# Optimization experiments

Hardware: AMD Instinct MI355X
Metric: run time of the kernel (lower is better)

## Reference

```python
import jax, jax.numpy as jnp
import numpy as np

H = 16      # how_many_heads
DH = 64     # dimension_of_head
D_K = 1024  # dimension_of_key (input dim); scaler = sqrt(D_K), faithful to source
NEG = -np.finfo(np.float32).max


def setup_inputs() -> dict:
    key0 = jax.random.key(0)
    ks = jax.random.split(key0, 8)
    B, S, D = 2, 2048, 1024
    query = jax.random.normal(ks[0], (B, S, D), dtype=jnp.float32)
    key_in = jax.random.normal(ks[1], (B, S, D), dtype=jnp.float32)
    value = jax.random.normal(ks[2], (B, S, D), dtype=jnp.float32)
    mask = jax.random.bernoulli(ks[3], 0.5, (B, S, S))  # bool, True = masked
    # nn.Linear(in, out, bias=False): y = x @ W^T with W:[out,in]; store [in,out] directly
    sc = 1.0 / np.sqrt(D)
    W_q = jax.random.normal(ks[4], (D, H * DH), dtype=jnp.float32) * sc
    W_k = jax.random.normal(ks[5], (D, H * DH), dtype=jnp.float32) * sc
    W_v = jax.random.normal(ks[6], (D, H * DH), dtype=jnp.float32) * sc
    W_o = jax.random.normal(ks[7], (H * DH, D), dtype=jnp.float32) * sc
    return {"query": query, "key": key_in, "value": value, "mask": mask,
            "W_q": W_q, "W_k": W_k, "W_v": W_v, "W_o": W_o}


def reference(query, key, value, mask, W_q, W_k, W_v, W_o):
    B, Sq, _ = query.shape
    # project and split heads: [B, S, H, DH] -> [B, H, S, DH]
    q = (query @ W_q).reshape(B, Sq, H, DH).transpose(0, 2, 1, 3)
    k = (key @ W_k).reshape(B, -1, H, DH).transpose(0, 2, 1, 3)
    v = (value @ W_v).reshape(B, -1, H, DH).transpose(0, 2, 1, 3)
    # scores: [B, H, Sq, Sk], scaled by sqrt(dimension_of_key)=sqrt(D_K)
    scores = jnp.einsum('bhqd,bhkd->bhqk', q, k) / np.float32(np.sqrt(D_K))
    # mask: [B, Sq, Sk] -> [B, H, Sq, Sk]; masked_fill with -finfo(float32).max
    scores = jnp.where(mask[:, None, :, :], NEG, scores)
    # FAITHFUL to source: softmax over dim=2 (the QUERY axis of the 4D tensor)
    attn = jax.nn.softmax(scores, axis=2)
    hidden = jnp.einsum('bhqk,bhkd->bhqd', attn, v)  # [B, H, Sq, DH]
    hidden = hidden.transpose(0, 2, 1, 3).reshape(B, Sq, H * DH) @ W_o
    return hidden, k, v
```

## Files before the change

### kernel.cpp

```cpp
#include <hip/hip_runtime.h>
#include <hip/hip_bf16.h>

#define BB 2
#define SS 2048
#define DD 1024
#define HH 16
#define DHH 64

#define SCLOG2E 0.045084221f

typedef unsigned short u16;
typedef unsigned int   u32;
typedef __bf16 bf16_t;
typedef bf16_t bf16x8 __attribute__((ext_vector_type(8)));
typedef u16    u16x8  __attribute__((ext_vector_type(8)));
typedef u32    u32x4v __attribute__((ext_vector_type(4)));
typedef float  f32x4  __attribute__((ext_vector_type(4)));

#define MFMA(a,b,c) __builtin_amdgcn_mfma_f32_16x16x32_bf16(a,b,c,0,0,0)

#define SW(c,r)  ((c) ^ ((r) & 7))
#define SW3(c,r) ((c) ^ ((r) & 3))

typedef __attribute__((address_space(1))) const unsigned int as1_u32;
typedef __attribute__((address_space(3))) unsigned int as3_u32;

__device__ __forceinline__ void gld16(const void* g, void* l){
  __builtin_amdgcn_global_load_lds((as1_u32*)g, (as3_u32*)l, 16, 0, 0);
}

__device__ __forceinline__ u16 f2bf(float f){
  u32 u = __builtin_bit_cast(u32, f);
  u32 r = (u + 0x7fffu + ((u >> 16) & 1u)) >> 16;
  return (u16)r;
}
__device__ __forceinline__ u16 nbf(float f){
  bf16_t b = (bf16_t)f;
  return __builtin_bit_cast(u16, b);
}
__device__ __forceinline__ float bf2f(u16 v){
  u32 u = ((u32)v) << 16;
  return __builtin_bit_cast(float, u);
}
__device__ __forceinline__ bf16x8 ldb8(const u16* p){
  return __builtin_bit_cast(bf16x8, *(const u16x8*)p);
}

__device__ __forceinline__ void stage64(const u16* __restrict__ g0, int stride,
                                        u16* lds0, int tid){
  int w = tid >> 6, lane = tid & 63;
  #pragma unroll
  for (int j = 0; j < 2; j++){
    int slot = j*256 + w*64 + lane;
    int row = slot >> 3, c = slot & 7;
    gld16(g0 + (size_t)row*stride + (SW(c,row) << 3),
          lds0 + (size_t)(j*256 + w*64)*8);
  }
}

__device__ __forceinline__ void stage32(const u16* __restrict__ g0, int stride,
                                        u16* lds0, int tid){
  int w = tid >> 6, lane = tid & 63;
  #pragma unroll
  for (int j = 0; j < 2; j++){
    int slot = j*256 + w*64 + lane;
    int row = slot >> 2, c = slot & 3;
    gld16(g0 + (size_t)row*stride + (SW3(c,row) << 3),
          lds0 + (size_t)(j*256 + w*64)*8);
  }
}

__global__ __launch_bounds__(256) void cvt3(const float* __restrict__ s0,
                                            const float* __restrict__ s1,
                                            const float* __restrict__ s2,
                                            u16* __restrict__ d0,
                                            u16* __restrict__ d1,
                                            u16* __restrict__ d2){
  const float* s = blockIdx.z == 0 ? s0 : (blockIdx.z == 1 ? s1 : s2);
  u16*         d = blockIdx.z == 0 ? d0 : (blockIdx.z == 1 ? d1 : d2);
  size_t i = ((size_t)blockIdx.x*256 + threadIdx.x) * 8;
  const float4* p = (const float4*)(s + i);
  float4 x = p[0], y = p[1];
  u16x8 u;
  u[0]=f2bf(x.x); u[1]=f2bf(x.y); u[2]=f2bf(x.z); u[3]=f2bf(x.w);
  u[4]=f2bf(y.x); u[5]=f2bf(y.y); u[6]=f2bf(y.z); u[7]=f2bf(y.w);
  *(u16x8*)(d + i) = u;
}

__global__ __launch_bounds__(256) void detect_mask(const u32* mw, u32* flag){
  __shared__ int fBig, fFloat;
  if (threadIdx.x == 0){ fBig = 0; fFloat = 0; }
  __syncthreads();
  for (int i = threadIdx.x; i < 4096; i += 256){
    u32 w = mw[i];
    if (w == 0x3f800000u) fFloat = 1;
    else if (w > 1u) fBig = 1;
  }
  __syncthreads();
  if (threadIdx.x == 0) *flag = fFloat ? 2u : (fBig ? 1u : 0u);
}

__global__ __launch_bounds__(256) void pack_mask(const void* __restrict__ mask,
                                                 const u32* __restrict__ flag,
                                                 u32* __restrict__ pm){
  int w = blockIdx.x * 256 + threadIdx.x;
  if (w >= BB*SS*(SS/32)) return;
  u32 f = *flag;
  size_t e0 = (size_t)w * 32;
  u32 bits = 0;
  if (f == 1u){
    const uchar4* mb = (const uchar4*)((const unsigned char*)mask + e0);
    #pragma unroll
    for (int j = 0; j < 8; j++){
      uchar4 v = mb[j];
      bits |= (v.x?1u:0u) << (4*j)   | (v.y?1u:0u) << (4*j+1)
            | (v.z?1u:0u) << (4*j+2) | (v.w?1u:0u) << (4*j+3);
    }
  } else if (f == 0u){
    const int4* mi = (const int4*)((const int*)mask + e0);
    #pragma unroll
    for (int j = 0; j < 8; j++){
      int4 v = mi[j];
      bits |= (v.x?1u:0u) << (4*j)   | (v.y?1u:0u) << (4*j+1)
            | (v.z?1u:0u) << (4*j+2) | (v.w?1u:0u) << (4*j+3);
    }
  } else {
    const float4* mf = (const float4*)((const float*)mask + e0);
    #pragma unroll
    for (int j = 0; j < 8; j++){
      float4 v = mf[j];
      bits |= (v.x!=0.f?1u:0u) << (4*j)   | (v.y!=0.f?1u:0u) << (4*j+1)
            | (v.z!=0.f?1u:0u) << (4*j+2) | (v.w!=0.f?1u:0u) << (4*j+3);
    }
  }
  pm[w] = bits;
}

__global__ __launch_bounds__(256) void prep_w(const float* __restrict__ W0,
                                              const float* __restrict__ W1,
                                              const float* __restrict__ W2,
                                              const float* __restrict__ W3,
                                              u16* __restrict__ Wt){
  const float* Ws[4] = {W0, W1, W2, W3};
  const float* W = Ws[blockIdx.z];
  float scl = (blockIdx.z == 0) ? SCLOG2E : 1.0f;
  u16* O = Wt + (size_t)blockIdx.z * DD * DD;
  __shared__ float tile[64][65];
  int kb = blockIdx.x * 64, nb = blockIdx.y * 64;
  int col = threadIdx.x & 63, rr = threadIdx.x >> 6;
  #pragma unroll
  for (int i = 0; i < 16; i++){
    int row = i*4 + rr;
    tile[row][col] = W[(size_t)(kb+row)*DD + nb + col];
  }
  __syncthreads();
  #pragma unroll
  for (int i = 0; i < 16; i++){
    int row = i*4 + rr;
    O[(size_t)(nb+row)*DD + kb + col] = f2bf(tile[col][row] * scl);
  }
}

struct GA { const u16* A; const u16* Bt; u16* Cb; float* Co; int mode; };

__global__ __launch_bounds__(256) void gemm32(GA a0, GA a1, GA a2){
  GA ga = blockIdx.z == 0 ? a0 : (blockIdx.z == 1 ? a1 : a2);
  __shared__ u16 As[2][128*32];
  __shared__ u16 Bs[2][128*32];
  int mb = blockIdx.x * 128, nb = blockIdx.y * 128;
  int tid = threadIdx.x, w = tid >> 6, lane = tid & 63, ln = lane & 15, g = lane >> 4;
  int wr = w >> 1, wc = w & 1;
  f32x4 acc[4][4];
  #pragma unroll
  for (int i = 0; i < 4; i++)
    #pragma unroll
    for (int j = 0; j < 4; j++) acc[i][j] = (f32x4){0,0,0,0};

  stage32(ga.A  + (size_t)mb*DD, DD, As[0], tid);
  stage32(ga.Bt + (size_t)nb*DD, DD, Bs[0], tid);
  __syncthreads();
  int buf = 0;
  for (int t = 0; t < 32; t++){
    if (t < 31){
      stage32(ga.A  + (size_t)mb*DD + (t+1)*32, DD, As[buf^1], tid);
      stage32(ga.Bt + (size_t)nb*DD + (t+1)*32, DD, Bs[buf^1], tid);
    }
    bf16x8 av[4], bv[4];
    #pragma unroll
    for (int mf = 0; mf < 4; mf++){
      int row = wr*64 + mf*16 + ln;
      av[mf] = ldb8(&As[buf][row*32 + (SW3(g,row) << 3)]);
    }
    #pragma unroll
    for (int nf = 0; nf < 4; nf++){
      int row = wc*64 + nf*16 + ln;
      bv[nf] = ldb8(&Bs[buf][row*32 + (SW3(g,row) << 3)]);
    }
    #pragma unroll
    for (int mf = 0; mf < 4; mf++)
      #pragma unroll
      for (int nf = 0; nf < 4; nf++)
        acc[mf][nf] = MFMA(av[mf], bv[nf], acc[mf][nf]);
    __syncthreads();
    buf ^= 1;
  }
  #pragma unroll
  for (int mf = 0; mf < 4; mf++){
    #pragma unroll
    for (int nf = 0; nf < 4; nf++){
      #pragma unroll
      for (int r = 0; r < 4; r++){
        int row = mb + wr*64 + mf*16 + g*4 + r;
        int col = nb + wc*64 + nf*16 + ln;
        float v = acc[mf][nf][r];
        if (ga.mode != 2)
          ga.Cb[(size_t)row*DD + col] = f2bf(v);
        if (ga.mode == 1){
          int b_ = row >> 11, s_ = row & (SS-1);
          int h_ = col >> 6,  d_ = col & 63;
          ga.Co[(((size_t)(b_*HH + h_))*SS + s_)*DHH + d_] = v;
        }
        if (ga.mode == 2)
          ga.Co[(size_t)row*DD + col] = v;
      }
    }
  }
}

__global__ __launch_bounds__(256) void pass1_sum(const u16* __restrict__ Qb,
                                                 const u16* __restrict__ Kb,
                                                 const u32* __restrict__ pm,
                                                 float* __restrict__ cO){
  __shared__ u16 Qst[2][64*64];
  int b = blockIdx.z, h = blockIdx.y;
  int kblk = blockIdx.x * 64;
  int tid = threadIdx.x, w = tid >> 6, lane = tid & 63, ln = lane & 15, g = lane >> 4;
  const u16* kp = Kb + ((size_t)b*SS + kblk + w*16 + ln)*DD + h*DHH + g*8;
  bf16x8 kf0 = ldb8(kp), kf1 = ldb8(kp + 32);
  float cr[4] = {0,0,0,0};

  stage64(Qb + ((size_t)b*SS)*DD + h*DHH, DD, Qst[0], tid);
  __syncthreads();
  int buf = 0;
  size_t kword = (size_t)(b*SS)*(SS/32) + ((kblk + w*16) >> 5);
  int ksh = (w & 1) * 16 + g*4;
  for (int t = 0; t < 32; t++){
    if (t < 31) stage64(Qb + ((size_t)b*SS + (t+1)*64)*DD + h*DHH, DD, Qst[buf^1], tid);
    #pragma unroll
    for (int qc = 0; qc < 4; qc++){
      int row = qc*16 + ln;
      bf16x8 b0 = ldb8(&Qst[buf][row*64 + (SW(g,  row) << 3)]);
      bf16x8 b1 = ldb8(&Qst[buf][row*64 + (SW(g+4,row) << 3)]);
      int q = t*64 + qc*16 + ln;
      f32x4 sf = {0,0,0,0};
      sf = MFMA(kf0, b0, sf);
      sf = MFMA(kf1, b1, sf);
      u32 mw = pm[(size_t)q*(SS/32) + kword];
      #pragma unroll
      for (int r = 0; r < 4; r++){
        float e = __builtin_amdgcn_exp2f(sf[r]);
        cr[r] += ((mw >> (ksh + r)) & 1u) ? 0.f : e;
      }
    }
    __syncthreads();
    buf ^= 1;
  }
  #pragma unroll
  for (int r = 0; r < 4; r++){
    #pragma unroll
    for (int msk = 1; msk < 16; msk <<= 1)
      cr[r] += __shfl_xor(cr[r], msk, 64);
  }
  if (ln == 0){
    #pragma unroll
    for (int r = 0; r < 4; r++)
      cO[((size_t)b*HH + h)*SS + kblk + w*16 + g*4 + r] = cr[r];
  }
}

__global__ __launch_bounds__(256) void scale_v(const u16* __restrict__ Vb,
                                               const float* __restrict__ cI,
                                               u16* __restrict__ Vt){
  int b = blockIdx.z, h = blockIdx.y;
  int st = blockIdx.x * 64;
  __shared__ u16 tile[64][72];
  int col = threadIdx.x & 63, rr = threadIdx.x >> 6;
  #pragma unroll
  for (int i = 0; i < 16; i++){
    int row = i*4 + rr;
    int s = st + row;
    float inv = 1.0f / cI[((size_t)b*HH + h)*SS + s];
    float v = bf2f(Vb[((size_t)b*SS + s)*DD + h*DHH + col]);
    tile[row][col] = f2bf(v * inv);
  }
  __syncthreads();
  int pc = (col & 32) + ((col >> 2) & 3)*8 + ((col >> 4) & 1)*4 + (col & 3);
  #pragma unroll
  for (int i = 0; i < 16; i++){
    int row = i*4 + rr;
    Vt[(((size_t)b*HH + h)*DHH + row)*SS + st + pc] = tile[col][row];
  }
}

__global__ __launch_bounds__(256) void pass2_pv(const u16* __restrict__ Qb,
                                                const u16* __restrict__ Kb,
                                                const u16* __restrict__ Vt,
                                                const u32* __restrict__ pm,
                                                u16* __restrict__ Hb){
  __shared__ u16 Kst[2][64*64];
  __shared__ u16 Vst[2][64*64];
  int b = blockIdx.z, h = blockIdx.y;
  int qt = blockIdx.x * 64;
  int tid = threadIdx.x, w = tid >> 6, lane = tid & 63, ln = lane & 15, g = lane >> 4;
  int qrow = qt + w*16 + ln;
  const u16* qp = Qb + ((size_t)b*SS + qrow)*DD + h*DHH + g*8;
  bf16x8 qf0 = ldb8(qp), qf1 = ldb8(qp + 32);
  f32x4 acc[4];
  #pragma unroll
  for (int d = 0; d < 4; d++) acc[d] = (f32x4){0,0,0,0};

  const u16* Kg  = Kb + ((size_t)b*SS)*DD + h*DHH;
  const u16* Vth = Vt + ((size_t)b*HH + h)*DHH*SS;
  const u32* pmrow = pm + ((size_t)b*SS + qrow)*(SS/32);

  stage64(Kg,  DD, Kst[0], tid);
  stage64(Vth, SS, Vst[0], tid);
  __syncthreads();
  int buf = 0;
  for (int t = 0; t < 32; t++){
    if (t < 31){
      stage64(Kg + (size_t)(t+1)*64*DD, DD, Kst[buf^1], tid);
      stage64(Vth + (t+1)*64,           SS, Vst[buf^1], tid);
    }
    u32 mlo = pmrow[t*2], mhi = pmrow[t*2 + 1];
    u32 pk[8];
    #pragma unroll
    for (int kc = 0; kc < 4; kc++){
      int row = kc*16 + ln;
      bf16x8 a0 = ldb8(&Kst[buf][row*64 + (SW(g,  row) << 3)]);
      bf16x8 a1 = ldb8(&Kst[buf][row*64 + (SW(g+4,row) << 3)]);
      f32x4 sf = {0,0,0,0};
      sf = MFMA(a0, qf0, sf);
      sf = MFMA(a1, qf1, sf);
      u32 mword = (kc < 2) ? mlo : mhi;
      int msh = (kc & 1) * 16 + g*4;
      float p0 = ((mword >> (msh+0)) & 1u) ? 0.f : __builtin_amdgcn_exp2f(sf[0]);
      float p1 = ((mword >> (msh+1)) & 1u) ? 0.f : __builtin_amdgcn_exp2f(sf[1]);
      float p2 = ((mword >> (msh+2)) & 1u) ? 0.f : __builtin_amdgcn_exp2f(sf[2]);
      float p3 = ((mword >> (msh+3)) & 1u) ? 0.f : __builtin_amdgcn_exp2f(sf[3]);
      pk[kc*2]   = (u32)nbf(p0) | ((u32)nbf(p1) << 16);
      pk[kc*2+1] = (u32)nbf(p2) | ((u32)nbf(p3) << 16);
    }
    #pragma unroll
    for (int kh = 0; kh < 2; kh++){
      bf16x8 pa = __builtin_bit_cast(bf16x8,
        (u32x4v){pk[4*kh], pk[4*kh+1], pk[4*kh+2], pk[4*kh+3]});
      #pragma unroll
      for (int df = 0; df < 4; df++){
        int row = df*16 + ln;
        bf16x8 bv = ldb8(&Vst[buf][row*64 + (SW(kh*4+g, row) << 3)]);
        acc[df] = MFMA(pa, bv, acc[df]);
      }
    }
    __syncthreads();
    buf ^= 1;
  }
  #pragma unroll
  for (int df = 0; df < 4; df++)
    #pragma unroll
    for (int r = 0; r < 4; r++){
      int row = qt + w*16 + g*4 + r;
      int col = h*DHH + df*16 + ln;
      Hb[((size_t)b*SS + row)*DD + col] = f2bf(acc[df][r]);
    }
}

extern "C" void kernel_launch(void* const* d_in, const int* in_sizes, int n_in,
                              void* d_out, int out_size, void* d_ws, size_t ws_size,
                              hipStream_t stream){
  (void)in_sizes; (void)n_in; (void)out_size; (void)ws_size;
  const float* query = (const float*)d_in[0];
  const float* key   = (const float*)d_in[1];
  const float* value = (const float*)d_in[2];
  const void*  mask  = d_in[3];
  const float* W_q = (const float*)d_in[4];
  const float* W_k = (const float*)d_in[5];
  const float* W_v = (const float*)d_in[6];
  const float* W_o = (const float*)d_in[7];

  float* out   = (float*)d_out;
  float* out_h = out;
  float* out_k = out   + (size_t)BB*HH*SS*DHH;
  float* out_v = out_k + (size_t)BB*HH*SS*DHH;

  char* w = (char*)d_ws;
  u16*   Wt  = (u16*)(w);
  u16*   Av  = (u16*)(w + (size_t)( 8u<<20));
  u16*   Qb  = (u16*)(w + (size_t)(16u<<20));
  u16*   Kb  = (u16*)(w + (size_t)(24u<<20));
  u16*   Vb  = (u16*)(w + (size_t)(32u<<20));
  u16*   Vt  = (u16*)(w + (size_t)(40u<<20));
  float* cS  = (float*)(w + (size_t)(48u<<20));
  u32*   pm  = (u32*)(w + (size_t)(48u<<20) + (512u<<10));
  u32*   flag= (u32*)(w + (size_t)(48u<<20) + (1664u<<10));
  u16*   Hb  = Av;
  u16*   Aq  = (u16*)out_h;
  u16*   Ak  = Aq + (size_t)BB*SS*DD;

  detect_mask<<<dim3(1), dim3(256), 0, stream>>>((const u32*)mask, flag);
  pack_mask<<<dim3(1024), dim3(256), 0, stream>>>(mask, flag, pm);
  prep_w<<<dim3(16,16,4), dim3(256), 0, stream>>>(W_q, W_k, W_v, W_o, Wt);

  cvt3<<<dim3(2048,1,3), dim3(256), 0, stream>>>(query, key, value, Aq, Ak, Av);

  GA gq = { Aq, Wt,             Qb, nullptr, 0 };
  GA gk = { Ak, Wt + 1*1048576, Kb, out_k,   1 };
  GA gv = { Av, Wt + 2*1048576, Vb, out_v,   1 };
  gemm32<<<dim3(32,8,3), dim3(256), 0, stream>>>(gq, gk, gv);

  pass1_sum<<<dim3(SS/64, HH, BB), dim3(256), 0, stream>>>(Qb, Kb, pm, cS);
  scale_v<<<dim3(SS/64, HH, BB), dim3(256), 0, stream>>>(Vb, cS, Vt);
  pass2_pv<<<dim3(SS/64, HH, BB), dim3(256), 0, stream>>>(Qb, Kb, Vt, pm, Hb);

  GA go = { Hb, Wt + 3*1048576, nullptr, out_h, 2 };
  gemm32<<<dim3(32,8,1), dim3(256), 0, stream>>>(go, go, go);
}
```

Measured before the change: 245.5 us.

## Deepen GEMM K-tile to 64 and double key rows per pass1 block

The projection and output GEMMs now stage 64-wide K slices instead of 32, which halves the number of loop iterations and barriers and doubles the MFMA work between syncs. The column-sum pass now handles 128 keys per block, with each wave holding two K fragments. Each staged Q tile and mask word is therefore reused for twice as many keys, halving Q re-streaming from global memory. The cost is more LDS per GEMM block (64 KB), more registers, and half as many pass1 blocks, which can reduce occupancy.

Result: faster. 229.8 us (-6.4%).

```diff
diff --git a/kernel.cpp b/kernel.cpp
--- a/kernel.cpp
+++ b/kernel.cpp
@@ -58,14 +58,14 @@
   }
 }
 
-__device__ __forceinline__ void stage32(const u16* __restrict__ g0, int stride,
-                                        u16* lds0, int tid){
+__device__ __forceinline__ void stage128(const u16* __restrict__ g0, int stride,
+                                         u16* lds0, int tid){
   int w = tid >> 6, lane = tid & 63;
   #pragma unroll
-  for (int j = 0; j < 2; j++){
+  for (int j = 0; j < 4; j++){
     int slot = j*256 + w*64 + lane;
-    int row = slot >> 2, c = slot & 3;
-    gld16(g0 + (size_t)row*stride + (SW3(c,row) << 3),
+    int row = slot >> 3, c = slot & 7;
+    gld16(g0 + (size_t)row*stride + (SW(c,row) << 3),
           lds0 + (size_t)(j*256 + w*64)*8);
   }
 }
@@ -163,10 +163,10 @@
 
 struct GA { const u16* A; const u16* Bt; u16* Cb; float* Co; int mode; };
 
-__global__ __launch_bounds__(256) void gemm32(GA a0, GA a1, GA a2){
+__global__ __launch_bounds__(256) void gemm64(GA a0, GA a1, GA a2){
   GA ga = blockIdx.z == 0 ? a0 : (blockIdx.z == 1 ? a1 : a2);
-  __shared__ u16 As[2][128*32];
-  __shared__ u16 Bs[2][128*32];
+  __shared__ u16 As[2][128*64];
+  __shared__ u16 Bs[2][128*64];
   int mb = blockIdx.x * 128, nb = blockIdx.y * 128;
   int tid = threadIdx.x, w = tid >> 6, lane = tid & 63, ln = lane & 15, g = lane >> 4;
   int wr = w >> 1, wc = w & 1;
@@ -176,31 +176,35 @@
     #pragma unroll
     for (int j = 0; j < 4; j++) acc[i][j] = (f32x4){0,0,0,0};
 
-  stage32(ga.A  + (size_t)mb*DD, DD, As[0], tid);
-  stage32(ga.Bt + (size_t)nb*DD, DD, Bs[0], tid);
+  stage128(ga.A  + (size_t)mb*DD, DD, As[0], tid);
+  stage128(ga.Bt + (size_t)nb*DD, DD, Bs[0], tid);
   __syncthreads();
   int buf = 0;
-  for (int t = 0; t < 32; t++){
-    if (t < 31){
-      stage32(ga.A  + (size_t)mb*DD + (t+1)*32, DD, As[buf^1], tid);
-      stage32(ga.Bt + (size_t)nb*DD + (t+1)*32, DD, Bs[buf^1], tid);
-    }
-    bf16x8 av[4], bv[4];
+  for (int t = 0; t < 16; t++){
+    if (t < 15){
+      stage128(ga.A  + (size_t)mb*DD + (t+1)*64, DD, As[buf^1], tid);
+      stage128(ga.Bt + (size_t)nb*DD + (t+1)*64, DD, Bs[buf^1], tid);
+    }
+    bf16x8 av[4][2], bv[4][2];
     #pragma unroll
     for (int mf = 0; mf < 4; mf++){
       int row = wr*64 + mf*16 + ln;
-      av[mf] = ldb8(&As[buf][row*32 + (SW3(g,row) << 3)]);
+      av[mf][0] = ldb8(&As[buf][row*64 + (SW(g,  row) << 3)]);
+      av[mf][1] = ldb8(&As[buf][row*64 + (SW(g+4,row) << 3)]);
     }
     #pragma unroll
     for (int nf = 0; nf < 4; nf++){
       int row = wc*64 + nf*16 + ln;
-      bv[nf] = ldb8(&Bs[buf][row*32 + (SW3(g,row) << 3)]);
+      bv[nf][0] = ldb8(&Bs[buf][row*64 + (SW(g,  row) << 3)]);
+      bv[nf][1] = ldb8(&Bs[buf][row*64 + (SW(g+4,row) << 3)]);
     }
     #pragma unroll
     for (int mf = 0; mf < 4; mf++)
       #pragma unroll
-      for (int nf = 0; nf < 4; nf++)
-        acc[mf][nf] = MFMA(av[mf], bv[nf], acc[mf][nf]);
+      for (int nf = 0; nf < 4; nf++){
+        acc[mf][nf] = MFMA(av[mf][0], bv[nf][0], acc[mf][nf]);
+        acc[mf][nf] = MFMA(av[mf][1], bv[nf][1], acc[mf][nf]);
+      }
     __syncthreads();
     buf ^= 1;
   }
@@ -233,17 +237,20 @@
                                                  float* __restrict__ cO){
   __shared__ u16 Qst[2][64*64];
   int b = blockIdx.z, h = blockIdx.y;
-  int kblk = blockIdx.x * 64;
+  int kblk = blockIdx.x * 128;
   int tid = threadIdx.x, w = tid >> 6, lane = tid & 63, ln = lane & 15, g = lane >> 4;
-  const u16* kp = Kb + ((size_t)b*SS + kblk + w*16 + ln)*DD + h*DHH + g*8;
-  bf16x8 kf0 = ldb8(kp), kf1 = ldb8(kp + 32);
-  float cr[4] = {0,0,0,0};
+  bf16x8 kf[2][2];
+  #pragma unroll
+  for (int f = 0; f < 2; f++){
+    const u16* kp = Kb + ((size_t)b*SS + kblk + w*32 + f*16 + ln)*DD + h*DHH + g*8;
+    kf[f][0] = ldb8(kp); kf[f][1] = ldb8(kp + 32);
+  }
+  float cr[2][4] = {{0,0,0,0},{0,0,0,0}};
 
   stage64(Qb + ((size_t)b*SS)*DD + h*DHH, DD, Qst[0], tid);
   __syncthreads();
   int buf = 0;
-  size_t kword = (size_t)(b*SS)*(SS/32) + ((kblk + w*16) >> 5);
-  int ksh = (w & 1) * 16 + g*4;
+  size_t kwbase = (size_t)(b*SS)*(SS/32) + (kblk >> 5) + w;
   for (int t = 0; t < 32; t++){
     if (t < 31) stage64(Qb + ((size_t)b*SS + (t+1)*64)*DD + h*DHH, DD, Qst[buf^1], tid);
     #pragma unroll
@@ -252,29 +259,36 @@
       bf16x8 b0 = ldb8(&Qst[buf][row*64 + (SW(g,  row) << 3)]);
       bf16x8 b1 = ldb8(&Qst[buf][row*64 + (SW(g+4,row) << 3)]);
       int q = t*64 + qc*16 + ln;
-      f32x4 sf = {0,0,0,0};
-      sf = MFMA(kf0, b0, sf);
-      sf = MFMA(kf1, b1, sf);
-      u32 mw = pm[(size_t)q*(SS/32) + kword];
-      #pragma unroll
-      for (int r = 0; r < 4; r++){
-        float e = __builtin_amdgcn_exp2f(sf[r]);
-        cr[r] += ((mw >> (ksh + r)) & 1u) ? 0.f : e;
+      u32 mw = pm[(size_t)q*(SS/32) + kwbase];
+      #pragma unroll
+      for (int f = 0; f < 2; f++){
+        f32x4 sf = {0,0,0,0};
+        sf = MFMA(kf[f][0], b0, sf);
+        sf = MFMA(kf[f][1], b1, sf);
+        #pragma unroll
+        for (int r = 0; r < 4; r++){
+          float e = __builtin_amdgcn_exp2f(sf[r]);
+          cr[f][r] += ((mw >> (f*16 + g*4 + r)) & 1u) ? 0.f : e;
+        }
       }
     }
     __syncthreads();
     buf ^= 1;
   }
   #pragma unroll
-  for (int r = 0; r < 4; r++){
-    #pragma unroll
-    for (int msk = 1; msk < 16; msk <<= 1)
-      cr[r] += __shfl_xor(cr[r], msk, 64);
-  }
+  for (int f = 0; f < 2; f++)
+    #pragma unroll
+    for (int r = 0; r < 4; r++){
+      #pragma unroll
+      for (int msk = 1; msk < 16; msk <<= 1)
+        cr[f][r] += __shfl_xor(cr[f][r], msk, 64);
+    }
   if (ln == 0){
     #pragma unroll
-    for (int r = 0; r < 4; r++)
-      cO[((size_t)b*HH + h)*SS + kblk + w*16 + g*4 + r] = cr[r];
+    for (int f = 0; f < 2; f++)
+      #pragma unroll
+      for (int r = 0; r < 4; r++)
+        cO[((size_t)b*HH + h)*SS + kblk + w*32 + f*16 + g*4 + r] = cr[f][r];
   }
 }
 
@@ -416,12 +430,12 @@
   GA gq = { Aq, Wt,             Qb, nullptr, 0 };
   GA gk = { Ak, Wt + 1*1048576, Kb, out_k,   1 };
   GA gv = { Av, Wt + 2*1048576, Vb, out_v,   1 };
-  gemm32<<<dim3(32,8,3), dim3(256), 0, stream>>>(gq, gk, gv);
-
-  pass1_sum<<<dim3(SS/64, HH, BB), dim3(256), 0, stream>>>(Qb, Kb, pm, cS);
+  gemm64<<<dim3(32,8,3), dim3(256), 0, stream>>>(gq, gk, gv);
+
+  pass1_sum<<<dim3(SS/128, HH, BB), dim3(256), 0, stream>>>(Qb, Kb, pm, cS);
   scale_v<<<dim3(SS/64, HH, BB), dim3(256), 0, stream>>>(Vb, cS, Vt);
   pass2_pv<<<dim3(SS/64, HH, BB), dim3(256), 0, stream>>>(Qb, Kb, Vt, pm, Hb);
 
   GA go = { Hb, Wt + 3*1048576, nullptr, out_h, 2 };
-  gemm32<<<dim3(32,8,1), dim3(256), 0, stream>>>(go, go, go);
-}
+  gemm64<<<dim3(32,8,1), dim3(256), 0, stream>>>(go, go, go);
+}
```

## Expand mask to 16-bit AND-masks, double pass1 key tile, raise PV priority

Applied to the files above, without the earlier changes.

Adds a kernel that expands the packed bit mask into per-element 16-bit all-ones/zero words, stored in the output buffer. pass2 can then zero masked probabilities with a bitwise AND instead of per-element bit extraction and select. pass1_sum now has each wave handle 32 keys instead of 16, reusing each staged Q fragment and mask word across two K fragments and halving the grid. s_setprio is raised around the PV MFMA block. The trade is a 16 MB mask expansion written and then re-read in pass2, plus an extra kernel launch.

After: 250.0 us. Within noise of the previous version (+1.9%).

```diff
diff --git a/kernel.cpp b/kernel.cpp
--- a/kernel.cpp
+++ b/kernel.cpp
@@ -14,6 +14,7 @@
 typedef __bf16 bf16_t;
 typedef bf16_t bf16x8 __attribute__((ext_vector_type(8)));
 typedef u16    u16x8  __attribute__((ext_vector_type(8)));
+typedef u32    u32x2v __attribute__((ext_vector_type(2)));
 typedef u32    u32x4v __attribute__((ext_vector_type(4)));
 typedef float  f32x4  __attribute__((ext_vector_type(4)));
 
@@ -136,6 +137,21 @@
   pm[w] = bits;
 }
 
+__global__ __launch_bounds__(256) void expand_mask(const u32* __restrict__ pm,
+                                                   u16* __restrict__ m16){
+  int w = blockIdx.x * 256 + threadIdx.x;
+  if (w >= BB*SS*(SS/32)) return;
+  u32 bits = pm[w];
+  #pragma unroll
+  for (int v = 0; v < 4; v++){
+    u16x8 o;
+    #pragma unroll
+    for (int j = 0; j < 8; j++)
+      o[j] = ((bits >> (v*8 + j)) & 1u) ? (u16)0 : (u16)0xFFFF;
+    *(u16x8*)(m16 + (size_t)w*32 + v*8) = o;
+  }
+}
+
 __global__ __launch_bounds__(256) void prep_w(const float* __restrict__ W0,
                                               const float* __restrict__ W1,
                                               const float* __restrict__ W2,
@@ -233,17 +249,20 @@
                                                  float* __restrict__ cO){
   __shared__ u16 Qst[2][64*64];
   int b = blockIdx.z, h = blockIdx.y;
-  int kblk = blockIdx.x * 64;
+  int kblk = blockIdx.x * 128;
   int tid = threadIdx.x, w = tid >> 6, lane = tid & 63, ln = lane & 15, g = lane >> 4;
-  const u16* kp = Kb + ((size_t)b*SS + kblk + w*16 + ln)*DD + h*DHH + g*8;
-  bf16x8 kf0 = ldb8(kp), kf1 = ldb8(kp + 32);
-  float cr[4] = {0,0,0,0};
+  bf16x8 kf[2][2];
+  #pragma unroll
+  for (int f = 0; f < 2; f++){
+    const u16* kp = Kb + ((size_t)b*SS + kblk + w*32 + f*16 + ln)*DD + h*DHH + g*8;
+    kf[f][0] = ldb8(kp); kf[f][1] = ldb8(kp + 32);
+  }
+  float cr[2][4] = {{0,0,0,0},{0,0,0,0}};
 
   stage64(Qb + ((size_t)b*SS)*DD + h*DHH, DD, Qst[0], tid);
   __syncthreads();
   int buf = 0;
-  size_t kword = (size_t)(b*SS)*(SS/32) + ((kblk + w*16) >> 5);
-  int ksh = (w & 1) * 16 + g*4;
+  size_t kwbase = (size_t)(b*SS)*(SS/32) + (kblk >> 5) + w;
   for (int t = 0; t < 32; t++){
     if (t < 31) stage64(Qb + ((size_t)b*SS + (t+1)*64)*DD + h*DHH, DD, Qst[buf^1], tid);
     #pragma unroll
@@ -252,29 +271,36 @@
       bf16x8 b0 = ldb8(&Qst[buf][row*64 + (SW(g,  row) << 3)]);
       bf16x8 b1 = ldb8(&Qst[buf][row*64 + (SW(g+4,row) << 3)]);
       int q = t*64 + qc*16 + ln;
-      f32x4 sf = {0,0,0,0};
-      sf = MFMA(kf0, b0, sf);
-      sf = MFMA(kf1, b1, sf);
-      u32 mw = pm[(size_t)q*(SS/32) + kword];
-      #pragma unroll
-      for (int r = 0; r < 4; r++){
-        float e = __builtin_amdgcn_exp2f(sf[r]);
-        cr[r] += ((mw >> (ksh + r)) & 1u) ? 0.f : e;
+      u32 mw = pm[(size_t)q*(SS/32) + kwbase];
+      #pragma unroll
+      for (int f = 0; f < 2; f++){
+        f32x4 sf = {0,0,0,0};
+        sf = MFMA(kf[f][0], b0, sf);
+        sf = MFMA(kf[f][1], b1, sf);
+        #pragma unroll
+        for (int r = 0; r < 4; r++){
+          float e = __builtin_amdgcn_exp2f(sf[r]);
+          cr[f][r] += ((mw >> (f*16 + g*4 + r)) & 1u) ? 0.f : e;
+        }
       }
     }
     __syncthreads();
     buf ^= 1;
   }
   #pragma unroll
-  for (int r = 0; r < 4; r++){
-    #pragma unroll
-    for (int msk = 1; msk < 16; msk <<= 1)
-      cr[r] += __shfl_xor(cr[r], msk, 64);
-  }
+  for (int f = 0; f < 2; f++)
+    #pragma unroll
+    for (int r = 0; r < 4; r++){
+      #pragma unroll
+      for (int msk = 1; msk < 16; msk <<= 1)
+        cr[f][r] += __shfl_xor(cr[f][r], msk, 64);
+    }
   if (ln == 0){
     #pragma unroll
-    for (int r = 0; r < 4; r++)
-      cO[((size_t)b*HH + h)*SS + kblk + w*16 + g*4 + r] = cr[r];
+    for (int f = 0; f < 2; f++)
+      #pragma unroll
+      for (int r = 0; r < 4; r++)
+        cO[((size_t)b*HH + h)*SS + kblk + w*32 + f*16 + g*4 + r] = cr[f][r];
   }
 }
 
@@ -305,7 +331,7 @@
 __global__ __launch_bounds__(256) void pass2_pv(const u16* __restrict__ Qb,
                                                 const u16* __restrict__ Kb,
                                                 const u16* __restrict__ Vt,
-                                                const u32* __restrict__ pm,
+                                                const u16* __restrict__ m16,
                                                 u16* __restrict__ Hb){
   __shared__ u16 Kst[2][64*64];
   __shared__ u16 Vst[2][64*64];
@@ -321,7 +347,7 @@
 
   const u16* Kg  = Kb + ((size_t)b*SS)*DD + h*DHH;
   const u16* Vth = Vt + ((size_t)b*HH + h)*DHH*SS;
-  const u32* pmrow = pm + ((size_t)b*SS + qrow)*(SS/32);
+  const u16* mrow = m16 + ((size_t)b*SS + qrow)*SS + g*4;
 
   stage64(Kg,  DD, Kst[0], tid);
   stage64(Vth, SS, Vst[0], tid);
@@ -332,7 +358,6 @@
       stage64(Kg + (size_t)(t+1)*64*DD, DD, Kst[buf^1], tid);
       stage64(Vth + (t+1)*64,           SS, Vst[buf^1], tid);
     }
-    u32 mlo = pmrow[t*2], mhi = pmrow[t*2 + 1];
     u32 pk[8];
     #pragma unroll
     for (int kc = 0; kc < 4; kc++){
@@ -342,15 +367,15 @@
       f32x4 sf = {0,0,0,0};
       sf = MFMA(a0, qf0, sf);
       sf = MFMA(a1, qf1, sf);
-      u32 mword = (kc < 2) ? mlo : mhi;
-      int msh = (kc & 1) * 16 + g*4;
-      float p0 = ((mword >> (msh+0)) & 1u) ? 0.f : __builtin_amdgcn_exp2f(sf[0]);
-      float p1 = ((mword >> (msh+1)) & 1u) ? 0.f : __builtin_amdgcn_exp2f(sf[1]);
-      float p2 = ((mword >> (msh+2)) & 1u) ? 0.f : __builtin_amdgcn_exp2f(sf[2]);
-      float p3 = ((mword >> (msh+3)) & 1u) ? 0.f : __builtin_amdgcn_exp2f(sf[3]);
-      pk[kc*2]   = (u32)nbf(p0) | ((u32)nbf(p1) << 16);
-      pk[kc*2+1] = (u32)nbf(p2) | ((u32)nbf(p3) << 16);
-    }
+      u32x2v mk = *(const u32x2v*)(mrow + t*64 + kc*16);
+      float p0 = __builtin_amdgcn_exp2f(sf[0]);
+      float p1 = __builtin_amdgcn_exp2f(sf[1]);
+      float p2 = __builtin_amdgcn_exp2f(sf[2]);
+      float p3 = __builtin_amdgcn_exp2f(sf[3]);
+      pk[kc*2]   = ((u32)nbf(p0) | ((u32)nbf(p1) << 16)) & mk[0];
+      pk[kc*2+1] = ((u32)nbf(p2) | ((u32)nbf(p3) << 16)) & mk[1];
+    }
+    __builtin_amdgcn_s_setprio(1);
     #pragma unroll
     for (int kh = 0; kh < 2; kh++){
       bf16x8 pa = __builtin_bit_cast(bf16x8,
@@ -362,6 +387,7 @@
         acc[df] = MFMA(pa, bv, acc[df]);
       }
     }
+    __builtin_amdgcn_s_setprio(0);
     __syncthreads();
     buf ^= 1;
   }
@@ -406,6 +432,7 @@
   u16*   Hb  = Av;
   u16*   Aq  = (u16*)out_h;
   u16*   Ak  = Aq + (size_t)BB*SS*DD;
+  u16*   m16 = (u16*)out_h;
 
   detect_mask<<<dim3(1), dim3(256), 0, stream>>>((const u32*)mask, flag);
   pack_mask<<<dim3(1024), dim3(256), 0, stream>>>(mask, flag, pm);
@@ -418,9 +445,11 @@
   GA gv = { Av, Wt + 2*1048576, Vb, out_v,   1 };
   gemm32<<<dim3(32,8,3), dim3(256), 0, stream>>>(gq, gk, gv);
 
-  pass1_sum<<<dim3(SS/64, HH, BB), dim3(256), 0, stream>>>(Qb, Kb, pm, cS);
+  expand_mask<<<dim3(1024), dim3(256), 0, stream>>>(pm, m16);
+
+  pass1_sum<<<dim3(SS/128, HH, BB), dim3(256), 0, stream>>>(Qb, Kb, pm, cS);
   scale_v<<<dim3(SS/64, HH, BB), dim3(256), 0, stream>>>(Vb, cS, Vt);
-  pass2_pv<<<dim3(SS/64, HH, BB), dim3(256), 0, stream>>>(Qb, Kb, Vt, pm, Hb);
+  pass2_pv<<<dim3(SS/64, HH, BB), dim3(256), 0, stream>>>(Qb, Kb, Vt, m16, Hb);
 
   GA go = { Hb, Wt + 3*1048576, nullptr, out_h, 2 };
   gemm32<<<dim3(32,8,1), dim3(256), 0, stream>>>(go, go, go);
```

## Double key columns per block in pass1 and remap blocks for XCD locality

Applied to the files above, without the earlier changes.

pass1_sum now handles 128 key columns per block (two 16-row K fragments per wave), so each staged Q tile and each packed mask word is reused for twice as much MFMA work and the grid halves. Both attention passes also remap the flat block index so that consecutive blocks on the same XCD (flat&7 grouping) share a (b,h) slice of Q/K/V, to improve L2 reuse. The cost is more registers per thread in pass1 and fewer blocks in flight to hide latency.

Measured after the change: 219.7 us. -10.5%, faster.

```diff
diff --git a/kernel.cpp b/kernel.cpp
--- a/kernel.cpp
+++ b/kernel.cpp
@@ -232,18 +232,24 @@
                                                  const u32* __restrict__ pm,
                                                  float* __restrict__ cO){
   __shared__ u16 Qst[2][64*64];
-  int b = blockIdx.z, h = blockIdx.y;
-  int kblk = blockIdx.x * 64;
+  int flat = blockIdx.x + (SS/128)*(blockIdx.y + HH*blockIdx.z);
+  int sw = (flat & 7)*64 + (flat >> 3);
+  int kblk = (sw & 15) * 128;
+  int rest = sw >> 4;
+  int h = rest & 15, b = rest >> 4;
   int tid = threadIdx.x, w = tid >> 6, lane = tid & 63, ln = lane & 15, g = lane >> 4;
-  const u16* kp = Kb + ((size_t)b*SS + kblk + w*16 + ln)*DD + h*DHH + g*8;
-  bf16x8 kf0 = ldb8(kp), kf1 = ldb8(kp + 32);
-  float cr[4] = {0,0,0,0};
+  bf16x8 kf[2][2];
+  #pragma unroll
+  for (int f = 0; f < 2; f++){
+    const u16* kp = Kb + ((size_t)b*SS + kblk + w*32 + f*16 + ln)*DD + h*DHH + g*8;
+    kf[f][0] = ldb8(kp); kf[f][1] = ldb8(kp + 32);
+  }
+  float cr[2][4] = {{0,0,0,0},{0,0,0,0}};
 
   stage64(Qb + ((size_t)b*SS)*DD + h*DHH, DD, Qst[0], tid);
   __syncthreads();
   int buf = 0;
-  size_t kword = (size_t)(b*SS)*(SS/32) + ((kblk + w*16) >> 5);
-  int ksh = (w & 1) * 16 + g*4;
+  size_t kwbase = (size_t)(b*SS)*(SS/32) + (kblk >> 5) + w;
   for (int t = 0; t < 32; t++){
     if (t < 31) stage64(Qb + ((size_t)b*SS + (t+1)*64)*DD + h*DHH, DD, Qst[buf^1], tid);
     #pragma unroll
@@ -252,29 +258,36 @@
       bf16x8 b0 = ldb8(&Qst[buf][row*64 + (SW(g,  row) << 3)]);
       bf16x8 b1 = ldb8(&Qst[buf][row*64 + (SW(g+4,row) << 3)]);
       int q = t*64 + qc*16 + ln;
-      f32x4 sf = {0,0,0,0};
-      sf = MFMA(kf0, b0, sf);
-      sf = MFMA(kf1, b1, sf);
-      u32 mw = pm[(size_t)q*(SS/32) + kword];
-      #pragma unroll
-      for (int r = 0; r < 4; r++){
-        float e = __builtin_amdgcn_exp2f(sf[r]);
-        cr[r] += ((mw >> (ksh + r)) & 1u) ? 0.f : e;
+      u32 mw = pm[(size_t)q*(SS/32) + kwbase];
+      #pragma unroll
+      for (int f = 0; f < 2; f++){
+        f32x4 sf = {0,0,0,0};
+        sf = MFMA(kf[f][0], b0, sf);
+        sf = MFMA(kf[f][1], b1, sf);
+        #pragma unroll
+        for (int r = 0; r < 4; r++){
+          float e = __builtin_amdgcn_exp2f(sf[r]);
+          cr[f][r] += ((mw >> (f*16 + g*4 + r)) & 1u) ? 0.f : e;
+        }
       }
     }
     __syncthreads();
     buf ^= 1;
   }
   #pragma unroll
-  for (int r = 0; r < 4; r++){
-    #pragma unroll
-    for (int msk = 1; msk < 16; msk <<= 1)
-      cr[r] += __shfl_xor(cr[r], msk, 64);
-  }
+  for (int f = 0; f < 2; f++)
+    #pragma unroll
+    for (int r = 0; r < 4; r++){
+      #pragma unroll
+      for (int msk = 1; msk < 16; msk <<= 1)
+        cr[f][r] += __shfl_xor(cr[f][r], msk, 64);
+    }
   if (ln == 0){
     #pragma unroll
-    for (int r = 0; r < 4; r++)
-      cO[((size_t)b*HH + h)*SS + kblk + w*16 + g*4 + r] = cr[r];
+    for (int f = 0; f < 2; f++)
+      #pragma unroll
+      for (int r = 0; r < 4; r++)
+        cO[((size_t)b*HH + h)*SS + kblk + w*32 + f*16 + g*4 + r] = cr[f][r];
   }
 }
 
@@ -309,8 +322,11 @@
                                                 u16* __restrict__ Hb){
   __shared__ u16 Kst[2][64*64];
   __shared__ u16 Vst[2][64*64];
-  int b = blockIdx.z, h = blockIdx.y;
-  int qt = blockIdx.x * 64;
+  int flat = blockIdx.x + (SS/64)*(blockIdx.y + HH*blockIdx.z);
+  int sw = (flat & 7)*128 + (flat >> 3);
+  int qt = (sw & 31) * 64;
+  int rest = sw >> 5;
+  int h = rest & 15, b = rest >> 4;
   int tid = threadIdx.x, w = tid >> 6, lane = tid & 63, ln = lane & 15, g = lane >> 4;
   int qrow = qt + w*16 + ln;
   const u16* qp = Qb + ((size_t)b*SS + qrow)*DD + h*DHH + g*8;
@@ -418,7 +434,7 @@
   GA gv = { Av, Wt + 2*1048576, Vb, out_v,   1 };
   gemm32<<<dim3(32,8,3), dim3(256), 0, stream>>>(gq, gk, gv);
 
-  pass1_sum<<<dim3(SS/64, HH, BB), dim3(256), 0, stream>>>(Qb, Kb, pm, cS);
+  pass1_sum<<<dim3(SS/128, HH, BB), dim3(256), 0, stream>>>(Qb, Kb, pm, cS);
   scale_v<<<dim3(SS/64, HH, BB), dim3(256), 0, stream>>>(Vb, cS, Vt);
   pass2_pv<<<dim3(SS/64, HH, BB), dim3(256), 0, stream>>>(Qb, Kb, Vt, pm, Hb);
 
```
